# Performance work log

Hardware: AMD Instinct MI355X
Metric: run time of the kernel (lower is better)

## Reference

```python
import jax, jax.numpy as jnp
import numpy as np

H = 16
ROPE_BASE = 10000.0

def _rope_cos_sin(seq_len, d_k, dtype):
    inv_freq = 1.0 / (ROPE_BASE ** (jnp.arange(0, d_k, 2, dtype=jnp.float32) / d_k))
    t = jnp.arange(seq_len, dtype=jnp.float32)
    freqs = jnp.einsum('s,d->sd', t, inv_freq)          # [S, d_k/2]
    emb = jnp.concatenate([freqs, freqs], axis=-1)       # [S, d_k]
    return jnp.cos(emb).astype(dtype), jnp.sin(emb).astype(dtype)

def _rotate_half(x):
    x1, x2 = jnp.split(x, 2, axis=-1)
    return jnp.concatenate([-x2, x1], axis=-1)

def setup_inputs() -> dict:
    key = jax.random.key(0)
    ks = jax.random.split(key, 11)
    B, S, D = 2, 2048, 1024
    sc = 0.02
    return {
        'query': jax.random.normal(ks[0], (B, S, D), jnp.float32),
        'key':   jax.random.normal(ks[1], (B, S, D), jnp.float32),
        'value': jax.random.normal(ks[2], (B, S, D), jnp.float32),
        'Wq': jax.random.normal(ks[3], (D, D), jnp.float32) * sc,
        'bq': jnp.zeros((D,), jnp.float32),
        'Wk': jax.random.normal(ks[4], (D, D), jnp.float32) * sc,
        'bk': jnp.zeros((D,), jnp.float32),
        'Wv': jax.random.normal(ks[5], (D, D), jnp.float32) * sc,
        'bv': jnp.zeros((D,), jnp.float32),
        'Wo': jax.random.normal(ks[6], (D, D), jnp.float32) * sc,
        'bo': jnp.zeros((D,), jnp.float32),
    }

def reference(query, key, value, Wq, bq, Wk, bk, Wv, bv, Wo, bo):
    B, S, D = query.shape
    d_k = D // H
    # QKV projections (torch Linear: x @ W.T + b), split heads -> [B, H, S, d_k]
    def proj(x, W, b):
        return (x @ W.T + b).reshape(B, S, H, d_k).transpose(0, 2, 1, 3)
    q = proj(query, Wq, bq)
    k = proj(key, Wk, bk)
    v = proj(value, Wv, bv)
    # Rotary position embedding applied to q and k
    cos, sin = _rope_cos_sin(S, d_k, q.dtype)            # [S, d_k]
    cos = cos[None, None, :, :]
    sin = sin[None, None, :, :]
    q = q * cos + _rotate_half(q) * sin
    k = k * cos + _rotate_half(k) * sin
    # Scaled dot-product attention
    scores = jnp.einsum('bhqd,bhkd->bhqk', q, k) / jnp.sqrt(jnp.asarray(d_k, q.dtype))
    attn = jax.nn.softmax(scores, axis=-1)
    x = jnp.einsum('bhqk,bhkd->bhqd', attn, v)           # [B, H, S, d_k]
    x = x.transpose(0, 2, 1, 3).reshape(B, S, D)
    return x @ Wo.T + bo
```

## Files before the change

### kernel.cpp

```cpp
#include <hip/hip_runtime.h>
#include <hip/hip_bf16.h>
#include <math.h>


#define B_ 2
#define S_ 2048
#define D_ 1024
#define H_ 16
#define DK 64

typedef __attribute__((ext_vector_type(8)))  __bf16    bf16x8;
typedef __attribute__((ext_vector_type(8)))  _Float16  f16x8;
typedef __attribute__((ext_vector_type(4)))  float     f32x4;
typedef __attribute__((ext_vector_type(16))) float     f32x16;
typedef __attribute__((ext_vector_type(8)))  unsigned short u16x8;
typedef __attribute__((ext_vector_type(4)))  unsigned short u16x4;

#if __has_builtin(__builtin_amdgcn_exp2f)
#define EXP2(x) __builtin_amdgcn_exp2f(x)
#else
#define EXP2(x) exp2f(x)
#endif

static __device__ __forceinline__ unsigned short f2bf(float x) {
    union { float f; unsigned u; } v; v.f = x;
    unsigned r = v.u + 0x7FFFu + ((v.u >> 16) & 1u);
    return (unsigned short)(r >> 16);
}
static __device__ __forceinline__ unsigned cvtpk(float lo, float hi) {
    unsigned r;
    asm("v_cvt_pk_bf16_f32 %0, %1, %2" : "=v"(r) : "v"(lo), "v"(hi));
    return r;
}
static __device__ __forceinline__ unsigned cvtpk16(float lo, float hi) {
    unsigned r;
    asm("v_cvt_pkrtz_f16_f32 %0, %1, %2" : "=v"(r) : "v"(lo), "v"(hi));
    return r;
}
static __device__ __forceinline__ void gload_lds16(const void* g, void* l) {
    __builtin_amdgcn_global_load_lds(
        (const __attribute__((address_space(1))) void*)g,
        (__attribute__((address_space(3))) void*)l, 16, 0, 0);
}
static __device__ __forceinline__ int swz(int R, int c) {
    return ((R >> 1) << 6) + (((((R & 1) << 2) | c) ^ ((R >> 1) & 7)) << 3);
}
union ffrag  { unsigned u[4]; f16x8  v; };
static __device__ __forceinline__ void splitpk16(float e0, float e1,
                                                 unsigned& hd, unsigned& ld) {
    hd = cvtpk16(e0, e1);
    union { unsigned u; _Float16 h[2]; } t; t.u = hd;
    ld = cvtpk16(e0 - (float)t.h[0], e1 - (float)t.h[1]);
}

__global__ __launch_bounds__(256) void wsplit4(
    const float* __restrict__ W0, const float* __restrict__ W1,
    const float* __restrict__ W2, const float* __restrict__ W3,
    unsigned short* __restrict__ out)
{
    const int idx = blockIdx.x * 256 + threadIdx.x;
    const int t = idx >> 17;
    const size_t e = (size_t)(idx & 131071) * 8;
    const float* src = (t==0 ? W0 : t==1 ? W1 : t==2 ? W2 : W3) + e;
    float4 a = *(const float4*)src;
    float4 b = *(const float4*)(src + 4);
    float x[8] = {a.x,a.y,a.z,a.w,b.x,b.y,b.z,b.w};
    union { _Float16 h[8]; u16x8 v; } Hh;
    #pragma unroll
    for (int j = 0; j < 8; ++j) Hh.h[j] = (_Float16)x[j];
    *(u16x8*)(out + (size_t)t * 1048576 + e) = Hh.v;
}

__global__ __launch_bounds__(512) void trigemm(
    const float* __restrict__ Aq, const float* __restrict__ Ak,
    const float* __restrict__ Av, const unsigned short* __restrict__ wsp,
    const float* __restrict__ bq, const float* __restrict__ bk,
    const float* __restrict__ bv,
    unsigned short* __restrict__ qb, unsigned short* __restrict__ kb,
    unsigned short* __restrict__ vt)
{
    __shared__ __align__(16) char ldsb[49152];
    const int pid = blockIdx.z;
    const float* A    = (pid==0) ? Aq : (pid==1) ? Ak : Av;
    const float* bias = (pid==0) ? bq : (pid==1) ? bk : bv;
    const unsigned short* Whp = wsp + (size_t)pid * 1048576;

    const int tid = threadIdx.x;
    const int w = tid >> 6, lane = tid & 63;
    const int l15 = lane & 15, g4 = lane >> 4;
    const int wr = w >> 1, wc = w & 1;
    const int bx = blockIdx.x, by = blockIdx.y;

    const int lr8 = lane >> 3;
    const int zz  = (lane & 7) ^ lr8;
    const float* gpA = A + (size_t)(bx*128 + w*32 + lr8) * 1024 + zz * 4;
    const int qq = w - 4;
    const int wR0 = qq*64 + (lr8 << 1) + (zz >> 2);
    const unsigned short* gpW = Whp + (size_t)(by*128 + wR0) * 1024 + (zz & 3) * 8;

    f32x4 acc[2][4];
    #pragma unroll
    for (int m = 0; m < 2; ++m)
        #pragma unroll
        for (int n = 0; n < 4; ++n) acc[m][n] = (f32x4){0.f,0.f,0.f,0.f};

    #define STAGE(T, BUF) do {                                               \
        if (w < 4) {                                                         \
            const float* g_ = gpA + (size_t)(T) * 32;                        \
            char* d_ = ldsb + (BUF)*24576 + w*4096;                          \
            gload_lds16(g_,          d_);                                    \
            gload_lds16(g_ + 8192,   d_ + 1024);                             \
            gload_lds16(g_ + 16384,  d_ + 2048);                             \
            gload_lds16(g_ + 24576,  d_ + 3072);                             \
        } else if (w < 6) {                                                  \
            const unsigned short* g_ = gpW + (size_t)(T) * 32;               \
            char* d_ = ldsb + (BUF)*24576 + 16384 + qq*4096;                 \
            gload_lds16(g_,          d_);                                    \
            gload_lds16(g_ + 16384,  d_ + 1024);                             \
            gload_lds16(g_ + 32768,  d_ + 2048);                             \
            gload_lds16(g_ + 49152,  d_ + 3072);                             \
        }                                                                    \
    } while (0)

    STAGE(0, 0);
    asm volatile("s_waitcnt vmcnt(0)" ::: "memory");
    __builtin_amdgcn_s_barrier();
    asm volatile("" ::: "memory");

    for (int t = 0; t < 32; ++t) {
        const int cur = t & 1;
        if (t < 31) {
            STAGE(t + 1, cur ^ 1);
            asm volatile("s_waitcnt vmcnt(4)" ::: "memory");
        } else {
            asm volatile("s_waitcnt vmcnt(0)" ::: "memory");
        }
        __builtin_amdgcn_s_barrier();
        asm volatile("" ::: "memory");

        const char* Abuf = ldsb + cur * 24576;
        const unsigned short* Whb = (const unsigned short*)(Abuf + 16384);

        ffrag ah[2];
        #pragma unroll
        for (int m = 0; m < 2; ++m) {
            const int R = wr*32 + m*16 + l15;
            const int b8 = R * 8, r7 = R & 7;
            f32x4 x0 = *(const f32x4*)(Abuf + (size_t)(b8 + ((g4*2)     ^ r7)) * 16);
            f32x4 x1 = *(const f32x4*)(Abuf + (size_t)(b8 + ((g4*2 + 1) ^ r7)) * 16);
            ah[m].u[0] = cvtpk16(x0[0], x0[1]);
            ah[m].u[1] = cvtpk16(x0[2], x0[3]);
            ah[m].u[2] = cvtpk16(x1[0], x1[1]);
            ah[m].u[3] = cvtpk16(x1[2], x1[3]);
        }
        f16x8 wh4[4];
        #pragma unroll
        for (int n = 0; n < 4; ++n) {
            const int off = swz(wc*64 + n*16 + l15, g4);
            wh4[n] = *(const f16x8*)(Whb + off);
        }
        #pragma unroll
        for (int m = 0; m < 2; ++m)
            #pragma unroll
            for (int n = 0; n < 4; ++n)
                acc[m][n] = __builtin_amdgcn_mfma_f32_16x16x32_f16(ah[m].v, wh4[n], acc[m][n], 0,0,0);

        asm volatile("" ::: "memory");
        __builtin_amdgcn_s_barrier();
        asm volatile("" ::: "memory");
    }
    #undef STAGE

    const int colBase = by*128 + wc*64;
    const int rowBase = bx*128 + wr*32;
    const int h = colBase >> 6;

    if (pid < 2) {
        unsigned short* Out = pid ? kb : qb;
        const float QSC = pid ? 1.0f : 0.125f * 1.44269504088896340736f;
        #pragma unroll
        for (int m = 0; m < 2; ++m) {
            const int srow0 = rowBase + m*16 + g4*4;
            const int b = srow0 >> 11;
            unsigned short* hb2 = Out + (size_t)(b*H_ + h) * S_ * DK;
            #pragma unroll
            for (int n = 0; n < 2; ++n) {
                const int d = n*16 + l15;
                const float invf = exp2f((float)d * -0.4152410118609203f);
                const float b1 = bias[h*64 + d], b2 = bias[h*64 + d + 32];
                #pragma unroll
                for (int r = 0; r < 4; ++r) {
                    const int s = (srow0 + r) & 2047;
                    const float x1 = acc[m][n][r]   + b1;
                    const float x2 = acc[m][n+2][r] + b2;
                    float sn, cc;
                    __sincosf((float)s * invf, &sn, &cc);
                    const float o1 = (x1*cc - x2*sn) * QSC;
                    const float o2 = (x2*cc + x1*sn) * QSC;
                    if (pid == 0) {
                        unsigned short* dst = hb2 + (size_t)s * DK;
                        dst[d]      = f2bf(o1);
                        dst[d + 32] = f2bf(o2);
                    } else {
                        unsigned short* tb = hb2 + (s >> 6) * 4096 + (s & 63) * 8;
                        tb[(d >> 3) * 512 + (d & 7)]        = f2bf(o1);
                        tb[(d >> 3) * 512 + 2048 + (d & 7)] = f2bf(o2);
                    }
                }
            }
        }
    } else {
        #pragma unroll
        for (int m = 0; m < 2; ++m) {
            const int srow0 = rowBase + m*16 + g4*4;
            const int b = srow0 >> 11, s0 = srow0 & 2047;
            unsigned short* tb = vt + (size_t)(b*H_ + h) * S_ * DK
                               + (s0 >> 6) * 4096 + ((s0 & 63) >> 3) * 512 + (s0 & 7);
            #pragma unroll
            for (int n = 0; n < 4; ++n) {
                const int d = n*16 + l15;
                const float bb = bias[h*64 + d];
                u16x4 pk;
                #pragma unroll
                for (int r = 0; r < 4; ++r) pk[r] = f2bf(acc[m][n][r] + bb);
                *(u16x4*)(tb + d * 8) = pk;
            }
        }
    }
}

__global__ __launch_bounds__(512) void mfma_gemm0(
    const unsigned short* __restrict__ Ah, const unsigned short* __restrict__ Al,
    const unsigned short* __restrict__ Wh,
    const float* __restrict__ bias, float* __restrict__ Out)
{
    __shared__ __align__(16) char ldsb[49152];
    const int tid = threadIdx.x;
    const int w = tid >> 6, lane = tid & 63;
    const int l15 = lane & 15, g4 = lane >> 4;
    const int wr = w >> 1, wc = w & 1;
    const int bx = blockIdx.x, by = blockIdx.y;

    const int u_ = w >> 1, qq = w & 1;
    const unsigned short* gsrc = (u_==0) ? Ah : (u_==1) ? Al : Wh;
    const int row0 = (u_ < 2) ? bx * 128 : by * 128;
    const int lr8 = lane >> 3;
    const int zz  = (lane & 7) ^ lr8;
    const int wR0 = qq*64 + (lr8 << 1) + (zz >> 2);
    const unsigned short* gp0 = gsrc + (size_t)(row0 + wR0) * 1024 + (zz & 3) * 8;

    f32x4 acc[2][4];
    #pragma unroll
    for (int m = 0; m < 2; ++m)
        #pragma unroll
        for (int n = 0; n < 4; ++n) acc[m][n] = (f32x4){0.f,0.f,0.f,0.f};

    #define STAGE(T, BUF) do {                                              \
        if (w < 6) {                                                        \
            const unsigned short* g_ = gp0 + (size_t)(T) * 32;              \
            char* d_ = ldsb + (BUF)*24576 + u_*8192 + qq*4096;              \
            gload_lds16(g_,          d_);                                   \
            gload_lds16(g_ + 16384,  d_ + 1024);                            \
            gload_lds16(g_ + 32768,  d_ + 2048);                            \
            gload_lds16(g_ + 49152,  d_ + 3072);                            \
        }                                                                   \
    } while (0)

    STAGE(0, 0);
    asm volatile("s_waitcnt vmcnt(0)" ::: "memory");
    __builtin_amdgcn_s_barrier();
    asm volatile("" ::: "memory");

    for (int t = 0; t < 32; ++t) {
        const int cur = t & 1;
        if (t < 31) {
            STAGE(t + 1, cur ^ 1);
            asm volatile("s_waitcnt vmcnt(4)" ::: "memory");
        } else {
            asm volatile("s_waitcnt vmcnt(0)" ::: "memory");
        }
        __builtin_amdgcn_s_barrier();
        asm volatile("" ::: "memory");

        const unsigned short* Ahb = (const unsigned short*)(ldsb + cur*24576);
        const unsigned short* Alb = Ahb + 4096;
        const unsigned short* Whb = Ahb + 8192;

        f16x8 ah2[2], al2[2], wh4[4];
        #pragma unroll
        for (int m = 0; m < 2; ++m) {
            const int off = swz(wr*32 + m*16 + l15, g4);
            ah2[m] = *(const f16x8*)(Ahb + off);
            al2[m] = *(const f16x8*)(Alb + off);
        }
        #pragma unroll
        for (int n = 0; n < 4; ++n) {
            const int off = swz(wc*64 + n*16 + l15, g4);
            wh4[n] = *(const f16x8*)(Whb + off);
        }
        #pragma unroll
        for (int m = 0; m < 2; ++m)
            #pragma unroll
            for (int n = 0; n < 4; ++n) {
                acc[m][n] = __builtin_amdgcn_mfma_f32_16x16x32_f16(ah2[m], wh4[n], acc[m][n], 0,0,0);
                acc[m][n] = __builtin_amdgcn_mfma_f32_16x16x32_f16(al2[m], wh4[n], acc[m][n], 0,0,0);
            }

        asm volatile("" ::: "memory");
        __builtin_amdgcn_s_barrier();
        asm volatile("" ::: "memory");
    }
    #undef STAGE

    const int colBase = by*128 + wc*64;
    const int rowBase = bx*128 + wr*32;
    #pragma unroll
    for (int m = 0; m < 2; ++m) {
        const int row = rowBase + m*16 + g4*4;
        #pragma unroll
        for (int n = 0; n < 4; ++n) {
            const int col = colBase + n*16 + l15;
            const float bb = bias[col];
            #pragma unroll
            for (int r = 0; r < 4; ++r)
                Out[(size_t)(row + r) * 1024 + col] = acc[m][n][r] + bb;
        }
    }
}

__global__ __launch_bounds__(512, 1) void attn_mfma8(
    const unsigned short* __restrict__ Qb, const unsigned short* __restrict__ Kb,
    const unsigned short* __restrict__ Vt,
    unsigned short* __restrict__ Xh, unsigned short* __restrict__ Xl)
{
    __shared__ __align__(16) char lds[65536];
    const unsigned bid = blockIdx.x;
    const int xcd = bid & 7, idx = bid >> 3;
    const int bh  = xcd * 4 + (idx >> 3);
    const int qt  = idx & 7;
    const int tid = threadIdx.x;
    const int w = tid >> 6, lane = tid & 63;
    const int l31 = lane & 31, hi = lane >> 5;
    const size_t bhO = (size_t)bh * S_ * DK;
    const int q0 = qt * 256 + w * 32;

    const int u0   = w * 4;
    const int isV  = u0 >> 4;
    const int u15  = u0 & 15;
    const int su0  = u15 >> 3;
    const unsigned short* sb = (isV ? Vt : Kb) + bhO;
    const int ch0 = u15 & 7;
    char* const dbase = lds;

    bf16x8 qf[4];
    #pragma unroll
    for (int ks = 0; ks < 4; ++ks)
        qf[ks] = *(const bf16x8*)(Qb + bhO + (size_t)(q0 + l31) * DK + ks*16 + hi*8);

    f32x16 oT[2];
    #pragma unroll
    for (int dh = 0; dh < 2; ++dh)
        #pragma unroll
        for (int r = 0; r < 16; ++r) oT[dh][r] = 0.f;
    float l_ = 0.f;

    #define ASTAGE(T, BUF) do {                                                     \
        const unsigned short* g_ = sb + (size_t)((T)*2 + su0) * 4096 + ch0 * 512    \
                                   + lane * 8;                                      \
        char* d_ = dbase + (BUF)*32768 + isV*16384 + su0*8192 + ch0*1024 + lane*16; \
        gload_lds16(g_,         d_);                                                \
        gload_lds16(g_ + 512,   d_ + 1024);                                         \
        gload_lds16(g_ + 1024,  d_ + 2048);                                         \
        gload_lds16(g_ + 1536,  d_ + 3072);                                         \
    } while (0)

    ASTAGE(0, 0);
    asm volatile("s_waitcnt vmcnt(0)" ::: "memory");
    __builtin_amdgcn_s_barrier();
    asm volatile("" ::: "memory");

    for (int t = 0; t < 16; ++t) {
        const int cur = t & 1;
        if (t < 15) {
            ASTAGE(t + 1, cur ^ 1);
            asm volatile("s_waitcnt vmcnt(4)" ::: "memory");
        } else {
            asm volatile("s_waitcnt vmcnt(0)" ::: "memory");
        }
        __builtin_amdgcn_s_barrier();
        asm volatile("" ::: "memory");

        const char* Kl = lds + cur * 32768;
        const char* Vl = Kl + 16384;

        f32x16 s2[4];
        __builtin_amdgcn_s_setprio(1);
        #pragma unroll
        for (int kb2 = 0; kb2 < 4; ++kb2) {
            f32x16 a;
            #pragma unroll
            for (int r = 0; r < 16; ++r) a[r] = 0.f;
            const char* kbase = Kl + (kb2 >> 1) * 8192 + ((kb2 & 1) * 32 + l31) * 16;
            #pragma unroll
            for (int ks = 0; ks < 4; ++ks) {
                bf16x8 kf = *(const bf16x8*)(kbase + (ks*2 + hi) * 1024);
                a = __builtin_amdgcn_mfma_f32_32x32x16_bf16(kf, qf[ks], a, 0, 0, 0);
            }
            s2[kb2] = a;
        }
        __builtin_amdgcn_s_setprio(0);

        {
            float lsum = 0.f;
            #pragma unroll
            for (int kb2 = 0; kb2 < 4; ++kb2)
                #pragma unroll
                for (int r = 0; r < 16; ++r) {
                    const float p = EXP2(s2[kb2][r]);
                    s2[kb2][r] = p; lsum += p;
                }
            l_ += lsum;
        }

        #pragma unroll
        for (int ks2 = 0; ks2 < 8; ++ks2) {
            const int kb2 = ks2 >> 1;
            const int R0  = (ks2 & 1) * 8;
            unsigned a0 = cvtpk(s2[kb2][R0+0], s2[kb2][R0+1]);
            unsigned a1 = cvtpk(s2[kb2][R0+2], s2[kb2][R0+3]);
            unsigned b0 = cvtpk(s2[kb2][R0+4], s2[kb2][R0+5]);
            unsigned b1 = cvtpk(s2[kb2][R0+6], s2[kb2][R0+7]);
            asm("v_permlane32_swap_b32 %0, %1" : "+v"(a0), "+v"(b0));
            asm("v_permlane32_swap_b32 %0, %1" : "+v"(a1), "+v"(b1));
            union { unsigned u[4]; bf16x8 v; } pf;
            pf.u[0] = a0; pf.u[1] = a1; pf.u[2] = b0; pf.u[3] = b1;
            const char* vbase = Vl + (ks2 >> 2) * 8192 + (((ks2 & 3) * 2) + hi) * 1024;
            __builtin_amdgcn_s_setprio(1);
            #pragma unroll
            for (int dh = 0; dh < 2; ++dh) {
                bf16x8 vf = *(const bf16x8*)(vbase + (dh*32 + l31) * 16);
                oT[dh] = __builtin_amdgcn_mfma_f32_32x32x16_bf16(vf, pf.v, oT[dh], 0, 0, 0);
            }
            __builtin_amdgcn_s_setprio(0);
        }

        asm volatile("" ::: "memory");
        __builtin_amdgcn_s_barrier();
        asm volatile("" ::: "memory");
    }
    #undef ASTAGE

    l_ += __shfl_xor(l_, 32, 64);
    const float inv = 1.0f / l_;
    const int b = bh >> 4, h = bh & 15;
    const int q = q0 + l31;
    unsigned short* xh = Xh + (((size_t)b * S_ + q) * H_ + h) * DK;
    unsigned short* xl = Xl + (((size_t)b * S_ + q) * H_ + h) * DK;
    #pragma unroll
    for (int dh = 0; dh < 2; ++dh)
        #pragma unroll
        for (int tt = 0; tt < 4; ++tt) {
            const int dk0 = dh*32 + tt*8 + hi*4;
            const float o0 = oT[dh][tt*4 + 0] * inv;
            const float o1 = oT[dh][tt*4 + 1] * inv;
            const float o2 = oT[dh][tt*4 + 2] * inv;
            const float o3 = oT[dh][tt*4 + 3] * inv;
            union { unsigned u[2]; u16x4 v; } hv, lv;
            splitpk16(o0, o1, hv.u[0], lv.u[0]);
            splitpk16(o2, o3, hv.u[1], lv.u[1]);
            *(u16x4*)(xh + dk0) = hv.v;
            *(u16x4*)(xl + dk0) = lv.v;
        }
}

extern "C" void kernel_launch(void* const* d_in, const int* in_sizes, int n_in,
                              void* d_out, int out_size, void* d_ws, size_t ws_size,
                              hipStream_t stream)
{
    const float* query = (const float*)d_in[0];
    const float* key   = (const float*)d_in[1];
    const float* value = (const float*)d_in[2];
    const float* Wq = (const float*)d_in[3];  const float* bq = (const float*)d_in[4];
    const float* Wk = (const float*)d_in[5];  const float* bk = (const float*)d_in[6];
    const float* Wv = (const float*)d_in[7];  const float* bv = (const float*)d_in[8];
    const float* Wo = (const float*)d_in[9];  const float* bo = (const float*)d_in[10];
    float* out = (float*)d_out;

    char* ws = (char*)d_ws;
    const size_t MB = (size_t)1 << 20;
    unsigned short* Xh  = (unsigned short*)(ws + 0*MB);
    unsigned short* Xl  = (unsigned short*)(ws + 8*MB);
    unsigned short* qb  = (unsigned short*)(ws + 16*MB);
    unsigned short* vt  = (unsigned short*)(ws + 24*MB);
    unsigned short* kb  = (unsigned short*)(ws + 40*MB);
    unsigned short* wsp = (unsigned short*)(ws + 48*MB);
    unsigned short* Woh = wsp + 3145728;

    wsplit4<<<2048, 256, 0, stream>>>(Wq, Wk, Wv, Wo, wsp);

    trigemm<<<dim3(32, 8, 3), 512, 0, stream>>>(query, key, value, wsp,
                                                bq, bk, bv, qb, kb, vt);

    attn_mfma8<<<256, 512, 0, stream>>>(qb, kb, vt, Xh, Xl);

    mfma_gemm0<<<dim3(32, 8), 512, 0, stream>>>(Xh, Xl, Woh, bo, out);
}
```

Measured before the change: 122.9 us.

## Convert A tile to fp16 via registers before LDS in QKV GEMM

The fp32 activation tile is now loaded into registers by all 512 threads, converted to fp16, and written to LDS in half precision. Before, direct global-to-LDS copies staged it as fp32 and every wave converted it again after each LDS read. This shrinks LDS use from 48KB to 32KB, halves A-fragment LDS reads, and spreads the load work across all waves. In exchange the conversion and LDS store run after the MFMAs in each iteration, and the loads now pass through registers.

```diff
diff --git a/kernel.cpp b/kernel.cpp
--- a/kernel.cpp
+++ b/kernel.cpp
@@ -79,7 +79,7 @@
     unsigned short* __restrict__ qb, unsigned short* __restrict__ kb,
     unsigned short* __restrict__ vt)
 {
-    __shared__ __align__(16) char ldsb[49152];
+    __shared__ __align__(16) char ldsb[32768];
     const int pid = blockIdx.z;
     const float* A    = (pid==0) ? Aq : (pid==1) ? Ak : Av;
     const float* bias = (pid==0) ? bq : (pid==1) ? bk : bv;
@@ -91,12 +91,14 @@
     const int wr = w >> 1, wc = w & 1;
     const int bx = blockIdx.x, by = blockIdx.y;
 
-    const int lr8 = lane >> 3;
-    const int zz  = (lane & 7) ^ lr8;
-    const float* gpA = A + (size_t)(bx*128 + w*32 + lr8) * 1024 + zz * 4;
-    const int qq = w - 4;
-    const int wR0 = qq*64 + (lr8 << 1) + (zz >> 2);
-    const unsigned short* gpW = Whp + (size_t)(by*128 + wR0) * 1024 + (zz & 3) * 8;
+    const int arow = tid >> 2, ac = tid & 3;
+    const float* gpA = A + (size_t)(bx*128 + arow) * 1024 + ac * 8;
+    const int aoff = swz(arow, ac);
+
+    const int sr_ = tid >> 3, slot_ = tid & 7;
+    const int z_  = slot_ ^ (sr_ & 7);
+    const int wR_ = sr_*2 + (z_ >> 2);
+    const unsigned short* gpW = Whp + (size_t)(by*128 + wR_) * 1024 + (z_ & 3) * 8;
 
     f32x4 acc[2][4];
     #pragma unroll
@@ -104,72 +106,58 @@
         #pragma unroll
         for (int n = 0; n < 4; ++n) acc[m][n] = (f32x4){0.f,0.f,0.f,0.f};
 
-    #define STAGE(T, BUF) do {                                               \
-        if (w < 4) {                                                         \
-            const float* g_ = gpA + (size_t)(T) * 32;                        \
-            char* d_ = ldsb + (BUF)*24576 + w*4096;                          \
-            gload_lds16(g_,          d_);                                    \
-            gload_lds16(g_ + 8192,   d_ + 1024);                             \
-            gload_lds16(g_ + 16384,  d_ + 2048);                             \
-            gload_lds16(g_ + 24576,  d_ + 3072);                             \
-        } else if (w < 6) {                                                  \
-            const unsigned short* g_ = gpW + (size_t)(T) * 32;               \
-            char* d_ = ldsb + (BUF)*24576 + 16384 + qq*4096;                 \
-            gload_lds16(g_,          d_);                                    \
-            gload_lds16(g_ + 16384,  d_ + 1024);                             \
-            gload_lds16(g_ + 32768,  d_ + 2048);                             \
-            gload_lds16(g_ + 49152,  d_ + 3072);                             \
-        }                                                                    \
-    } while (0)
-
-    STAGE(0, 0);
-    asm volatile("s_waitcnt vmcnt(0)" ::: "memory");
+    {
+        float4 p0 = *(const float4*)(gpA);
+        float4 p1 = *(const float4*)(gpA + 4);
+        gload_lds16(gpW, ldsb + 8192 + tid * 16);
+        union { unsigned u[4]; u16x8 v; } hh;
+        hh.u[0] = cvtpk16(p0.x, p0.y); hh.u[1] = cvtpk16(p0.z, p0.w);
+        hh.u[2] = cvtpk16(p1.x, p1.y); hh.u[3] = cvtpk16(p1.z, p1.w);
+        *(u16x8*)((unsigned short*)ldsb + aoff) = hh.v;
+    }
+    asm volatile("s_waitcnt vmcnt(0) lgkmcnt(0)" ::: "memory");
     __builtin_amdgcn_s_barrier();
     asm volatile("" ::: "memory");
 
     for (int t = 0; t < 32; ++t) {
         const int cur = t & 1;
+        float4 n0, n1;
         if (t < 31) {
-            STAGE(t + 1, cur ^ 1);
-            asm volatile("s_waitcnt vmcnt(4)" ::: "memory");
+            n0 = *(const float4*)(gpA + (t+1)*32);
+            n1 = *(const float4*)(gpA + (t+1)*32 + 4);
+            gload_lds16(gpW + (size_t)(t+1)*32, ldsb + (cur^1)*16384 + 8192 + tid*16);
+            asm volatile("s_waitcnt vmcnt(3)" ::: "memory");
         } else {
             asm volatile("s_waitcnt vmcnt(0)" ::: "memory");
         }
         __builtin_amdgcn_s_barrier();
         asm volatile("" ::: "memory");
 
-        const char* Abuf = ldsb + cur * 24576;
-        const unsigned short* Whb = (const unsigned short*)(Abuf + 16384);
-
-        ffrag ah[2];
-        #pragma unroll
-        for (int m = 0; m < 2; ++m) {
-            const int R = wr*32 + m*16 + l15;
-            const int b8 = R * 8, r7 = R & 7;
-            f32x4 x0 = *(const f32x4*)(Abuf + (size_t)(b8 + ((g4*2)     ^ r7)) * 16);
-            f32x4 x1 = *(const f32x4*)(Abuf + (size_t)(b8 + ((g4*2 + 1) ^ r7)) * 16);
-            ah[m].u[0] = cvtpk16(x0[0], x0[1]);
-            ah[m].u[1] = cvtpk16(x0[2], x0[3]);
-            ah[m].u[2] = cvtpk16(x1[0], x1[1]);
-            ah[m].u[3] = cvtpk16(x1[2], x1[3]);
-        }
-        f16x8 wh4[4];
-        #pragma unroll
-        for (int n = 0; n < 4; ++n) {
-            const int off = swz(wc*64 + n*16 + l15, g4);
-            wh4[n] = *(const f16x8*)(Whb + off);
-        }
+        const unsigned short* Ab = (const unsigned short*)(ldsb + cur*16384);
+        const unsigned short* Wb = Ab + 4096;
+        f16x8 ah[2], wh4[4];
         #pragma unroll
         for (int m = 0; m < 2; ++m)
+            ah[m] = *(const f16x8*)(Ab + swz(wr*32 + m*16 + l15, g4));
+        #pragma unroll
+        for (int n = 0; n < 4; ++n)
+            wh4[n] = *(const f16x8*)(Wb + swz(wc*64 + n*16 + l15, g4));
+        #pragma unroll
+        for (int m = 0; m < 2; ++m)
             #pragma unroll
             for (int n = 0; n < 4; ++n)
-                acc[m][n] = __builtin_amdgcn_mfma_f32_16x16x32_f16(ah[m].v, wh4[n], acc[m][n], 0,0,0);
-
-        asm volatile("" ::: "memory");
-        __builtin_amdgcn_s_barrier();
-        asm volatile("" ::: "memory");
-    }
-    #undef STAGE
+                acc[m][n] = __builtin_amdgcn_mfma_f32_16x16x32_f16(ah[m], wh4[n], acc[m][n], 0,0,0);
+
+        if (t < 31) {
+            union { unsigned u[4]; u16x8 v; } hh;
+            hh.u[0] = cvtpk16(n0.x, n0.y); hh.u[1] = cvtpk16(n0.z, n0.w);
+            hh.u[2] = cvtpk16(n1.x, n1.y); hh.u[3] = cvtpk16(n1.z, n1.w);
+            *(u16x8*)((unsigned short*)(ldsb + (cur^1)*16384) + aoff) = hh.v;
+        }
+        asm volatile("s_waitcnt lgkmcnt(0)" ::: "memory");
+        __builtin_amdgcn_s_barrier();
+        asm volatile("" ::: "memory");
+    }
 
     const int colBase = by*128 + wc*64;
     const int rowBase = bx*128 + wr*32;
```

Measured after the change: 117.9 us. -4.1%, faster.
